# Optimization experiments

Measured on AMD Instinct MI355X. Metric: run time of the kernel, lower is better.

Reference implementation:

```python
import jax, jax.numpy as jnp
import numpy as np

B = 262144
IN_F = 64
OUT_F = 64
HID = 256
QUAT_IDX = np.array([0, 1, 2, 3])
NON_QUAT_IDX = np.array(sorted(set(range(OUT_F)) - set(QUAT_IDX.tolist())))
TRIU_R, TRIU_C = np.triu_indices(4)  # row-major order, matches torch.triu_indices


def setup_inputs() -> dict:
    key = jax.random.key(0)
    k0, k1, k2 = jax.random.split(key, 3)
    z = jax.random.normal(k0, (B, IN_F), dtype=jnp.float32)
    W1 = jax.random.normal(k1, (IN_F, HID), dtype=jnp.float32) * (1.0 / np.sqrt(IN_F))
    b1 = jnp.zeros((HID,), dtype=jnp.float32)
    W2 = jax.random.normal(k2, (HID, OUT_F - 4), dtype=jnp.float32) * (1.0 / np.sqrt(HID))
    b2 = jnp.zeros((OUT_F - 4,), dtype=jnp.float32)
    return {"z": z, "W1": W1, "b1": b1, "W2": W2, "b2": b2}


def _recover_quat(z_v):
    # z_v: (B, 10) -> symmetric M: (B, 4, 4)
    n = z_v.shape[0]
    M = jnp.zeros((n, 4, 4), dtype=z_v.dtype)
    M = M.at[:, TRIU_R, TRIU_C].set(z_v)
    M = M.at[:, TRIU_C, TRIU_R].set(z_v)  # symmetrize (diagonal rewritten identically)
    _, vecs = jnp.linalg.eigh(M)  # ascending eigenvalues
    q = vecs[:, :, -1]            # eigenvector of largest eigenvalue, (B, 4)
    sign = jnp.sign(q[:, 0:1])
    sign = jnp.where(sign == 0, jnp.ones_like(sign), sign)
    sign = jax.lax.stop_gradient(sign)
    return q * sign


def reference(z, W1, b1, W2, b2):
    z2 = z.reshape(-1, z.shape[-1])
    q_pred = _recover_quat(z2[:, :10])
    h = jax.nn.relu(z2 @ W1 + b1)
    others_pred = h @ W2 + b2
    x = jnp.zeros((z2.shape[0], OUT_F), dtype=z2.dtype)
    x = x.at[:, QUAT_IDX].set(q_pred)
    x = x.at[:, NON_QUAT_IDX].set(others_pred)
    return x.reshape(*z.shape[:-1], OUT_F)
```

## Files before the change

kernel.cpp:

```cpp
#include <hip/hip_runtime.h>
#include <stdint.h>

#define NROWS 262144
#define INF   64
#define HIDN  256
#define OUTM  60
#define BLOCKS 512
#define BLOCK  512

typedef __attribute__((ext_vector_type(8))) short bf16x8;
typedef __attribute__((ext_vector_type(4))) float f32x4;

__device__ __forceinline__ uint32_t pk2(float lo, float hi) {
  uint32_t r;
  asm("v_cvt_pk_bf16_f32 %0, %1, %2" : "=v"(r) : "v"(lo), "v"(hi));
  return r;
}

union U8 { uint32_t u[4]; bf16x8 v; uint4 q; };

__global__ __launch_bounds__(BLOCK, 2)
void veronese_fused(const float* __restrict__ z,  const float* __restrict__ W1,
                    const float* __restrict__ b1, const float* __restrict__ W2,
                    const float* __restrict__ b2, float* __restrict__ out) {
  __shared__ __align__(16) uint8_t lds[65536];
  const int tid = threadIdx.x;

  {
    const int hid  = tid & 255;
    const int half = tid >> 8;
    #pragma unroll
    for (int cc = 0; cc < 4; ++cc) {
      const int hc = half * 4 + cc;
      float f[8];
      #pragma unroll
      for (int j = 0; j < 8; ++j) f[j] = W1[(hc*8 + j) * HIDN + hid];
      U8 u;
      u.u[0] = pk2(f[0], f[1]); u.u[1] = pk2(f[2], f[3]);
      u.u[2] = pk2(f[4], f[5]); u.u[3] = pk2(f[6], f[7]);
      uint32_t off = (uint32_t)hid * 128 + (uint32_t)((hc * 16) ^ ((hid & 7) << 4));
      *reinterpret_cast<uint4*>(lds + off) = u.q;
    }
  }
  {
    const int o   = tid & 63;
    const int seg = tid >> 6;
    #pragma unroll
    for (int uu = 0; uu < 4; ++uu) {
      const int hb = seg * 32 + uu * 8;
      float f[8];
      #pragma unroll
      for (int j = 0; j < 8; ++j)
        f[j] = (o >= 4) ? W2[(hb + j) * OUTM + (o - 4)] : 0.0f;
      U8 u;
      u.u[0] = pk2(f[0], f[1]); u.u[1] = pk2(f[2], f[3]);
      u.u[2] = pk2(f[4], f[5]); u.u[3] = pk2(f[6], f[7]);
      uint32_t off = 32768u + (uint32_t)o * 512 + (uint32_t)((hb * 2) ^ ((o & 7) << 4));
      *reinterpret_cast<uint4*>(lds + off) = u.q;
    }
  }
  __syncthreads();

  const int l   = tid & 63;
  const int w   = tid >> 6;
  const int g   = l >> 4;
  const int l15 = l & 15;
  const uint32_t swz = (uint32_t)((l & 7) << 4);
  const int srcA = l15 + 32*(g & 1) + 16*(g >> 1);
  const int srcB = l15 + 32*(g & 1) + 16*(1 - (g >> 1));
  const bool hiq = (g & 2) != 0;
  const bool amI16 = (l & 16) != 0;

  f32x4 bias2[4];
  #pragma unroll
  for (int m = 0; m < 4; ++m) {
    int ob = 16*m + 4*g;
    if (ob >= 4) bias2[m] = *reinterpret_cast<const f32x4*>(b2 + ob - 4);
    else         bias2[m] = (f32x4){0.f, 0.f, 0.f, 0.f};
  }

  const int rowBase = blockIdx.x * BLOCK + w * 64;

  const float* zq = z + (size_t)(rowBase + l) * INF;
  float4 qv0 = reinterpret_cast<const float4*>(zq)[0];
  float4 qv1 = reinterpret_cast<const float4*>(zq)[1];
  float4 qv2 = reinterpret_cast<const float4*>(zq)[2];

  bf16x8 zf[4][2];
  #pragma unroll
  for (int t = 0; t < 4; ++t) {
    const float* zp = z + (size_t)(rowBase + 16*t + l15) * INF;
    #pragma unroll
    for (int k1 = 0; k1 < 2; ++k1) {
      float4 a0 = *reinterpret_cast<const float4*>(zp + k1*32 + 8*g);
      float4 a1 = *reinterpret_cast<const float4*>(zp + k1*32 + 8*g + 4);
      U8 u;
      u.u[0] = pk2(a0.x, a0.y); u.u[1] = pk2(a0.z, a0.w);
      u.u[2] = pk2(a1.x, a1.y); u.u[3] = pk2(a1.z, a1.w);
      zf[t][k1] = u.v;
    }
  }

  float q0, q1, q2, q3;
  {
    float zv[10] = {qv0.x,qv0.y,qv0.z,qv0.w, qv1.x,qv1.y,qv1.z,qv1.w,
                    qv2.x,qv2.y};
    float M[4][4];
    M[0][0]=zv[0]; M[0][1]=zv[1]; M[0][2]=zv[2]; M[0][3]=zv[3];
    M[1][1]=zv[4]; M[1][2]=zv[5]; M[1][3]=zv[6];
    M[2][2]=zv[7]; M[2][3]=zv[8]; M[3][3]=zv[9];
    M[1][0]=zv[1]; M[2][0]=zv[2]; M[3][0]=zv[3];
    M[2][1]=zv[5]; M[3][1]=zv[6]; M[3][2]=zv[8];
    float V[4][4] = {{1.f,0.f,0.f,0.f},{0.f,1.f,0.f,0.f},
                     {0.f,0.f,1.f,0.f},{0.f,0.f,0.f,1.f}};

#define JROT(p, q) do {                                                      \
    float apq = M[p][q];                                                     \
    float app = M[p][p], aqq = M[q][q];                                      \
    float tau = (aqq - app) * (0.5f * __builtin_amdgcn_rcpf(apq));           \
    float t_r = copysignf(1.0f, tau) *                                       \
        __builtin_amdgcn_rcpf(fabsf(tau) +                                   \
            __builtin_amdgcn_sqrtf(fmaf(tau, tau, 1.0f)));                   \
    float t   = (fabsf(apq) > 1e-25f) ? t_r : 0.0f;                          \
    float c   = __builtin_amdgcn_rsqf(fmaf(t, t, 1.0f));                     \
    float s   = t * c;                                                       \
    M[p][p] = fmaf(-t, apq, app);                                            \
    M[q][q] = fmaf( t, apq, aqq);                                            \
    M[p][q] = 0.0f; M[q][p] = 0.0f;                                          \
    _Pragma("unroll")                                                        \
    for (int r = 0; r < 4; ++r) {                                            \
      if (r != p && r != q) {                                                \
        float arp = M[r][p], arq = M[r][q];                                  \
        float nrp = fmaf(-s, arq, c * arp);                                  \
        float nrq = fmaf( s, arp, c * arq);                                  \
        M[r][p] = nrp; M[p][r] = nrp;                                        \
        M[r][q] = nrq; M[q][r] = nrq;                                        \
      }                                                                      \
    }                                                                        \
    _Pragma("unroll")                                                        \
    for (int r = 0; r < 4; ++r) {                                            \
      float vrp = V[r][p], vrq = V[r][q];                                    \
      V[r][p] = fmaf(-s, vrq, c * vrp);                                      \
      V[r][q] = fmaf( s, vrp, c * vrq);                                      \
    }                                                                        \
  } while (0)

    #pragma unroll
    for (int sweep = 0; sweep < 6; ++sweep) {
      JROT(0, 1); JROT(0, 2); JROT(0, 3);
      JROT(1, 2); JROT(1, 3); JROT(2, 3);
    }
#undef JROT

    float bv = M[0][0];
    q0 = V[0][0]; q1 = V[1][0]; q2 = V[2][0]; q3 = V[3][0];
    #pragma unroll
    for (int j = 1; j < 4; ++j) {
      float dj = M[j][j];
      bool  b  = dj > bv;
      bv = b ? dj      : bv;
      q0 = b ? V[0][j] : q0;
      q1 = b ? V[1][j] : q1;
      q2 = b ? V[2][j] : q2;
      q3 = b ? V[3][j] : q3;
    }
    float sgn = (q0 < 0.0f) ? -1.0f : 1.0f;
    q0 *= sgn; q1 *= sgn; q2 *= sgn; q3 *= sgn;
  }

  f32x4 acc2[4][4];
  #pragma unroll
  for (int t = 0; t < 4; ++t)
    #pragma unroll
    for (int m = 0; m < 4; ++m) acc2[t][m] = bias2[m];

  for (int ks = 0; ks < 8; ++ks) {
    uint32_t c[4][4];
    #pragma unroll
    for (int mm = 0; mm < 2; ++mm) {
      const int hb = 16*(2*ks + mm) + 4*g;
      f32x4 bv = *reinterpret_cast<const f32x4*>(b1 + hb);
      uint32_t rowb = (uint32_t)(16*(2*ks+mm) + l15) * 128;
      bf16x8 a0 = *reinterpret_cast<const bf16x8*>(
          lds + rowb + (((uint32_t)(16*g)) ^ swz));
      bf16x8 a1 = *reinterpret_cast<const bf16x8*>(
          lds + rowb + (((uint32_t)(64 + 16*g)) ^ swz));
      f32x4 acc1[4];
      __builtin_amdgcn_s_setprio(1);
      #pragma unroll
      for (int t = 0; t < 4; ++t) {
        acc1[t] = __builtin_amdgcn_mfma_f32_16x16x32_bf16(a0, zf[t][0], bv, 0,0,0);
        acc1[t] = __builtin_amdgcn_mfma_f32_16x16x32_bf16(a1, zf[t][1], acc1[t], 0,0,0);
      }
      __builtin_amdgcn_s_setprio(0);
      #pragma unroll
      for (int t = 0; t < 4; ++t) {
        float h0 = fmaxf(acc1[t][0], 0.f), h1 = fmaxf(acc1[t][1], 0.f);
        float h2 = fmaxf(acc1[t][2], 0.f), h3 = fmaxf(acc1[t][3], 0.f);
        c[t][2*mm+0] = pk2(h0, h1);
        c[t][2*mm+1] = pk2(h2, h3);
      }
    }
    bf16x8 a2[4];
    #pragma unroll
    for (int m = 0; m < 4; ++m) {
      uint32_t rowb = 32768u + (uint32_t)(16*m + l15) * 512;
      a2[m] = *reinterpret_cast<const bf16x8*>(
          lds + rowb + (((uint32_t)(64*ks + 16*g)) ^ swz));
    }
    #pragma unroll
    for (int t = 0; t < 4; ++t) {
      uint32_t v02a = amI16 ? c[t][2] : c[t][0];
      uint32_t v13a = amI16 ? c[t][3] : c[t][1];
      uint32_t v02b = amI16 ? c[t][0] : c[t][2];
      uint32_t v13b = amI16 ? c[t][1] : c[t][3];
      uint32_t s0 = (uint32_t)__shfl((int)v02a, srcA, 64);
      uint32_t s1 = (uint32_t)__shfl((int)v13a, srcA, 64);
      uint32_t s2 = (uint32_t)__shfl((int)v02b, srcB, 64);
      uint32_t s3 = (uint32_t)__shfl((int)v13b, srcB, 64);
      U8 bu;
      bu.u[0] = hiq ? s2 : s0;
      bu.u[1] = hiq ? s3 : s1;
      bu.u[2] = hiq ? s0 : s2;
      bu.u[3] = hiq ? s1 : s3;
      __builtin_amdgcn_s_setprio(1);
      #pragma unroll
      for (int m = 0; m < 4; ++m)
        acc2[t][m] = __builtin_amdgcn_mfma_f32_16x16x32_bf16(a2[m], bu.v, acc2[t][m], 0,0,0);
      __builtin_amdgcn_s_setprio(0);
    }
  }

  #pragma unroll
  for (int t = 0; t < 4; ++t) {
    int src = 16*t + l15;
    float v0 = __shfl(q0, src, 64);
    float v1 = __shfl(q1, src, 64);
    float v2 = __shfl(q2, src, 64);
    float v3 = __shfl(q3, src, 64);
    if (g == 0) {
      acc2[t][0][0] = v0; acc2[t][0][1] = v1;
      acc2[t][0][2] = v2; acc2[t][0][3] = v3;
    }
  }

  #pragma unroll
  for (int t = 0; t < 4; ++t) {
    float* op = out + (size_t)(rowBase + 16*t + l15) * 64;
    #pragma unroll
    for (int m = 0; m < 4; ++m) {
      float4 v = make_float4(acc2[t][m][0], acc2[t][m][1],
                             acc2[t][m][2], acc2[t][m][3]);
      *reinterpret_cast<float4*>(op + 16*m + 4*g) = v;
    }
  }
}

extern "C" void kernel_launch(void* const* d_in, const int* in_sizes, int n_in,
                              void* d_out, int out_size, void* d_ws, size_t ws_size,
                              hipStream_t stream) {
  const float* z  = (const float*)d_in[0];
  const float* W1 = (const float*)d_in[1];
  const float* b1 = (const float*)d_in[2];
  const float* W2 = (const float*)d_in[3];
  const float* b2 = (const float*)d_in[4];
  float* out = (float*)d_out;

  hipLaunchKernelGGL(veronese_fused, dim3(BLOCKS), dim3(BLOCK), 0, stream,
                     z, W1, b1, W2, b2, out);
}
```

Measured before the change: 151.5 us.

## Use 1024-thread blocks with 32 rows per wave and LDS-shared quaternion results

Doubles the block to 1024 threads while keeping 512 rows per block, so each wave handles 32 rows (two MFMA row tiles) instead of 64. The Jacobi eigen-solve runs only on the first 8 waves (64 rows each), and its quaternions are passed to the writing waves through an extra 8 KB LDS region behind a barrier. The goal is more waves per CU to hide latency and fewer registers per thread. In exchange, each LDS tile of W1/W2 is reused across fewer rows per wave, a block-wide sync is added, and the eigen-solve work is unevenly split across waves.

Result: faster. 141.2 us (-6.8%).

```diff
diff --git a/kernel.cpp b/kernel.cpp
--- a/kernel.cpp
+++ b/kernel.cpp
@@ -6,7 +6,7 @@
 #define HIDN  256
 #define OUTM  60
 #define BLOCKS 512
-#define BLOCK  512
+#define BLOCK  1024
 
 typedef __attribute__((ext_vector_type(8))) short bf16x8;
 typedef __attribute__((ext_vector_type(4))) float f32x4;
@@ -19,19 +19,19 @@
 
 union U8 { uint32_t u[4]; bf16x8 v; uint4 q; };
 
-__global__ __launch_bounds__(BLOCK, 2)
+__global__ __launch_bounds__(BLOCK, 1)
 void veronese_fused(const float* __restrict__ z,  const float* __restrict__ W1,
                     const float* __restrict__ b1, const float* __restrict__ W2,
                     const float* __restrict__ b2, float* __restrict__ out) {
-  __shared__ __align__(16) uint8_t lds[65536];
+  __shared__ __align__(16) uint8_t lds[65536 + 8192];
   const int tid = threadIdx.x;
 
   {
-    const int hid  = tid & 255;
-    const int half = tid >> 8;
-    #pragma unroll
-    for (int cc = 0; cc < 4; ++cc) {
-      const int hc = half * 4 + cc;
+    const int hid = tid & 255;
+    const int q4  = tid >> 8;
+    #pragma unroll
+    for (int cc = 0; cc < 2; ++cc) {
+      const int hc = q4 * 2 + cc;
       float f[8];
       #pragma unroll
       for (int j = 0; j < 8; ++j) f[j] = W1[(hc*8 + j) * HIDN + hid];
@@ -46,8 +46,8 @@
     const int o   = tid & 63;
     const int seg = tid >> 6;
     #pragma unroll
-    for (int uu = 0; uu < 4; ++uu) {
-      const int hb = seg * 32 + uu * 8;
+    for (int uu = 0; uu < 2; ++uu) {
+      const int hb = seg * 16 + uu * 8;
       float f[8];
       #pragma unroll
       for (int j = 0; j < 8; ++j)
@@ -79,16 +79,12 @@
     else         bias2[m] = (f32x4){0.f, 0.f, 0.f, 0.f};
   }
 
-  const int rowBase = blockIdx.x * BLOCK + w * 64;
-
-  const float* zq = z + (size_t)(rowBase + l) * INF;
-  float4 qv0 = reinterpret_cast<const float4*>(zq)[0];
-  float4 qv1 = reinterpret_cast<const float4*>(zq)[1];
-  float4 qv2 = reinterpret_cast<const float4*>(zq)[2];
-
-  bf16x8 zf[4][2];
-  #pragma unroll
-  for (int t = 0; t < 4; ++t) {
+  const int blockRow = blockIdx.x * (BLOCK / 2);
+  const int rowBase  = blockRow + w * 32;
+
+  bf16x8 zf[2][2];
+  #pragma unroll
+  for (int t = 0; t < 2; ++t) {
     const float* zp = z + (size_t)(rowBase + 16*t + l15) * INF;
     #pragma unroll
     for (int k1 = 0; k1 < 2; ++k1) {
@@ -101,8 +97,11 @@
     }
   }
 
-  float q0, q1, q2, q3;
-  {
+  if (w < 8) {
+    const float* zq = z + (size_t)(blockRow + w * 64 + l) * INF;
+    float4 qv0 = reinterpret_cast<const float4*>(zq)[0];
+    float4 qv1 = reinterpret_cast<const float4*>(zq)[1];
+    float4 qv2 = reinterpret_cast<const float4*>(zq)[2];
     float zv[10] = {qv0.x,qv0.y,qv0.z,qv0.w, qv1.x,qv1.y,qv1.z,qv1.w,
                     qv2.x,qv2.y};
     float M[4][4];
@@ -153,7 +152,7 @@
 #undef JROT
 
     float bv = M[0][0];
-    q0 = V[0][0]; q1 = V[1][0]; q2 = V[2][0]; q3 = V[3][0];
+    float q0 = V[0][0], q1 = V[1][0], q2 = V[2][0], q3 = V[3][0];
     #pragma unroll
     for (int j = 1; j < 4; ++j) {
       float dj = M[j][j];
@@ -165,17 +164,18 @@
       q3 = b ? V[3][j] : q3;
     }
     float sgn = (q0 < 0.0f) ? -1.0f : 1.0f;
-    q0 *= sgn; q1 *= sgn; q2 *= sgn; q3 *= sgn;
-  }
-
-  f32x4 acc2[4][4];
-  #pragma unroll
-  for (int t = 0; t < 4; ++t)
+    float4 qq = make_float4(q0*sgn, q1*sgn, q2*sgn, q3*sgn);
+    *reinterpret_cast<float4*>(lds + 65536 + (uint32_t)(w*64 + l) * 16) = qq;
+  }
+
+  f32x4 acc2[2][4];
+  #pragma unroll
+  for (int t = 0; t < 2; ++t)
     #pragma unroll
     for (int m = 0; m < 4; ++m) acc2[t][m] = bias2[m];
 
   for (int ks = 0; ks < 8; ++ks) {
-    uint32_t c[4][4];
+    uint32_t c[2][4];
     #pragma unroll
     for (int mm = 0; mm < 2; ++mm) {
       const int hb = 16*(2*ks + mm) + 4*g;
@@ -185,16 +185,16 @@
           lds + rowb + (((uint32_t)(16*g)) ^ swz));
       bf16x8 a1 = *reinterpret_cast<const bf16x8*>(
           lds + rowb + (((uint32_t)(64 + 16*g)) ^ swz));
-      f32x4 acc1[4];
+      f32x4 acc1[2];
       __builtin_amdgcn_s_setprio(1);
       #pragma unroll
-      for (int t = 0; t < 4; ++t) {
+      for (int t = 0; t < 2; ++t) {
         acc1[t] = __builtin_amdgcn_mfma_f32_16x16x32_bf16(a0, zf[t][0], bv, 0,0,0);
         acc1[t] = __builtin_amdgcn_mfma_f32_16x16x32_bf16(a1, zf[t][1], acc1[t], 0,0,0);
       }
       __builtin_amdgcn_s_setprio(0);
       #pragma unroll
-      for (int t = 0; t < 4; ++t) {
+      for (int t = 0; t < 2; ++t) {
         float h0 = fmaxf(acc1[t][0], 0.f), h1 = fmaxf(acc1[t][1], 0.f);
         float h2 = fmaxf(acc1[t][2], 0.f), h3 = fmaxf(acc1[t][3], 0.f);
         c[t][2*mm+0] = pk2(h0, h1);
@@ -209,7 +209,7 @@
           lds + rowb + (((uint32_t)(64*ks + 16*g)) ^ swz));
     }
     #pragma unroll
-    for (int t = 0; t < 4; ++t) {
+    for (int t = 0; t < 2; ++t) {
       uint32_t v02a = amI16 ? c[t][2] : c[t][0];
       uint32_t v13a = amI16 ? c[t][3] : c[t][1];
       uint32_t v02b = amI16 ? c[t][0] : c[t][2];
@@ -231,21 +231,18 @@
     }
   }
 
-  #pragma unroll
-  for (int t = 0; t < 4; ++t) {
-    int src = 16*t + l15;
-    float v0 = __shfl(q0, src, 64);
-    float v1 = __shfl(q1, src, 64);
-    float v2 = __shfl(q2, src, 64);
-    float v3 = __shfl(q3, src, 64);
+  __syncthreads();
+  #pragma unroll
+  for (int t = 0; t < 2; ++t) {
     if (g == 0) {
-      acc2[t][0][0] = v0; acc2[t][0][1] = v1;
-      acc2[t][0][2] = v2; acc2[t][0][3] = v3;
-    }
-  }
-
-  #pragma unroll
-  for (int t = 0; t < 4; ++t) {
+      f32x4 qv = *reinterpret_cast<const f32x4*>(
+          lds + 65536 + (uint32_t)(w*32 + 16*t + l15) * 16);
+      acc2[t][0] = qv;
+    }
+  }
+
+  #pragma unroll
+  for (int t = 0; t < 2; ++t) {
     float* op = out + (size_t)(rowBase + 16*t + l15) * 64;
     #pragma unroll
     for (int m = 0; m < 4; ++m) {
```
